# Kernel tuning notes

Measured on AMD Instinct MI355X. Metric: run time of the kernel, lower is better.

The kernel has to match this reference:

```python
import jax, jax.numpy as jnp
import numpy as np

EPS = 1e-12  # matches torch F.normalize eps

def _l2norm(v, axis):
    n = jnp.sqrt(jnp.sum(v * v, axis=axis, keepdims=True))
    return v / jnp.maximum(n, EPS)

def setup_inputs() -> dict:
    key = jax.random.key(0)
    k1, k2, k3 = jax.random.split(key, 3)
    N, D, H, W, K = 64, 128, 60, 80, 64
    x = jax.random.normal(k1, (N, D, H, W), dtype=jnp.float32)
    conv_w = jax.random.normal(k2, (K, D), dtype=jnp.float32) * 0.1
    centroids = jax.random.uniform(k3, (K, D), dtype=jnp.float32)
    return {"x": x, "conv_w": conv_w, "centroids": centroids}

def reference(x, conv_w, centroids):
    N, D, H, W = x.shape
    K = conv_w.shape[0]
    # descriptor-wise L2 normalization over channel dim
    x = _l2norm(x, axis=1)
    xf = x.reshape(N, D, H * W)                       # [N, D, P]
    # 1x1 conv (no bias) == matmul over channels, then softmax over clusters
    logits = jnp.einsum('kd,ndp->nkp', conv_w, xf)    # [N, K, P]
    sa = jax.nn.softmax(logits, axis=1)               # [N, K, P]
    # vlad[n,k,:] = sum_p sa[n,k,p] * (xf[n,:,p] - centroids[k])
    agg = jnp.einsum('nkp,ndp->nkd', sa, xf)          # [N, K, D]
    vlad = agg - sa.sum(axis=-1)[..., None] * centroids[None]
    vlad = _l2norm(vlad, axis=2)                      # intra-normalization
    vlad = vlad.reshape(N, K * D)
    vlad = _l2norm(vlad, axis=1)                      # global L2 norm
    return vlad
```

## Files before the change

### kernel.cpp

```cpp
#include <hip/hip_runtime.h>
#include <math.h>

#define NN 64
#define DD 128
#define PP 4800
#define KK 64
#define BPN 15
#define PB  320
#define CP  64
#define NCH 5

#define WT  136
#define XPT 136
#define XDT 88
#define SAT 88

typedef __attribute__((ext_vector_type(8))) short bf16x8;
typedef __attribute__((ext_vector_type(4))) float f32x4;

__device__ __forceinline__ unsigned short f2bf(float f) {
  unsigned u = __float_as_uint(f);
  u += 0x7fffu + ((u >> 16) & 1u);
  return (unsigned short)(u >> 16);
}
__device__ __forceinline__ float bf2f(unsigned short s) {
  return __uint_as_float(((unsigned)s) << 16);
}

template <bool ATOMIC>
__global__ __launch_bounds__(256, 2) void main_kernel(const float* __restrict__ x,
                                                      const float* __restrict__ conv_w,
                                                      float* __restrict__ pagg,
                                                      float* __restrict__ pssum) {
  __shared__ __align__(16) unsigned short w_s[KK * WT];
  __shared__ __align__(16) unsigned short xpd[CP * XPT];
  __shared__ __align__(16) unsigned short xdp[DD * XDT];
  __shared__ __align__(16) unsigned short sa_s[KK * SAT];
  __shared__ float invn_s[CP];
  __shared__ float ssred[256];

  const int b = blockIdx.x;
  const int n = b / BPN;
  const int sl = b % BPN;
  const int t = threadIdx.x;
  const int lane = t & 63;
  const int wv = t >> 6;
  const int lq = lane >> 4;
  const int ll = lane & 15;

  {
    int k = t >> 2, h = t & 3;
    const float4* wp = (const float4*)(conv_w + k * DD + h * 32);
    unsigned short* dst = &w_s[k * WT + h * 32];
#pragma unroll
    for (int i = 0; i < 4; ++i) {
      float4 a = wp[2 * i], c = wp[2 * i + 1];
      bf16x8 o = {(short)f2bf(a.x), (short)f2bf(a.y), (short)f2bf(a.z), (short)f2bf(a.w),
                  (short)f2bf(c.x), (short)f2bf(c.y), (short)f2bf(c.z), (short)f2bf(c.w)};
      *(bf16x8*)&dst[8 * i] = o;
    }
  }

  f32x4 acc[8];
#pragma unroll
  for (int i = 0; i < 8; ++i) acc[i] = (f32x4){0.f, 0.f, 0.f, 0.f};
  float ssacc[16];
#pragma unroll
  for (int i = 0; i < 16; ++i) ssacc[i] = 0.f;

  for (int c = 0; c < NCH; ++c) {
    const int p0 = sl * PB + c * CP;
    __syncthreads();

    {
      int d = t >> 1, h = t & 1;
      const float4* xp = (const float4*)(x + ((size_t)n * DD + d) * PP + p0 + h * 32);
      unsigned short* xdrow = &xdp[d * XDT + h * 32];
#pragma unroll
      for (int i = 0; i < 4; ++i) {
        float4 a = xp[2 * i], c2 = xp[2 * i + 1];
        unsigned short e0 = f2bf(a.x), e1 = f2bf(a.y), e2 = f2bf(a.z), e3 = f2bf(a.w);
        unsigned short e4 = f2bf(c2.x), e5 = f2bf(c2.y), e6 = f2bf(c2.z), e7 = f2bf(c2.w);
        bf16x8 o = {(short)e0, (short)e1, (short)e2, (short)e3,
                    (short)e4, (short)e5, (short)e6, (short)e7};
        *(bf16x8*)&xdrow[8 * i] = o;
        int pl = h * 32 + 8 * i;
        xpd[(pl + 0) * XPT + d] = e0;
        xpd[(pl + 1) * XPT + d] = e1;
        xpd[(pl + 2) * XPT + d] = e2;
        xpd[(pl + 3) * XPT + d] = e3;
        xpd[(pl + 4) * XPT + d] = e4;
        xpd[(pl + 5) * XPT + d] = e5;
        xpd[(pl + 6) * XPT + d] = e6;
        xpd[(pl + 7) * XPT + d] = e7;
      }
    }
    __syncthreads();

    if (t < 128) {
      int p = t >> 1, hh = t & 1;
      const unsigned short* row = &xpd[p * XPT + hh * 64];
      float s = 0.f;
#pragma unroll
      for (int i = 0; i < 8; ++i) {
        bf16x8 v = *(const bf16x8*)&row[8 * i];
#pragma unroll
        for (int j = 0; j < 8; ++j) {
          float f = bf2f((unsigned short)v[j]);
          s = fmaf(f, f, s);
        }
      }
      s += __shfl_xor(s, 1);
      if (hh == 0) invn_s[p] = 1.0f / fmaxf(sqrtf(s), 1e-12f);
    }
    __syncthreads();

    {
      f32x4 lg[4];
#pragma unroll
      for (int kt = 0; kt < 4; ++kt) lg[kt] = (f32x4){0.f, 0.f, 0.f, 0.f};
#pragma unroll
      for (int ks = 0; ks < 4; ++ks) {
        bf16x8 bfrag = *(const bf16x8*)&xpd[(wv * 16 + ll) * XPT + ks * 32 + lq * 8];
#pragma unroll
        for (int kt = 0; kt < 4; ++kt) {
          bf16x8 afrag = *(const bf16x8*)&w_s[(kt * 16 + ll) * WT + ks * 32 + lq * 8];
          lg[kt] = __builtin_amdgcn_mfma_f32_16x16x32_bf16(afrag, bfrag, lg[kt], 0, 0, 0);
        }
      }
      float iv = invn_s[wv * 16 + ll];
      float vals[16];
      float m = -1e30f;
#pragma unroll
      for (int kt = 0; kt < 4; ++kt)
#pragma unroll
        for (int r = 0; r < 4; ++r) {
          float v = lg[kt][r] * iv;
          vals[kt * 4 + r] = v;
          m = fmaxf(m, v);
        }
      m = fmaxf(m, __shfl_xor(m, 16));
      m = fmaxf(m, __shfl_xor(m, 32));
      float se = 0.f;
#pragma unroll
      for (int i = 0; i < 16; ++i) {
        float e = __expf(vals[i] - m);
        vals[i] = e;
        se += e;
      }
      se += __shfl_xor(se, 16);
      se += __shfl_xor(se, 32);
      float rinv = 1.0f / se;
      float r2 = rinv * iv;
#pragma unroll
      for (int kt = 0; kt < 4; ++kt)
#pragma unroll
        for (int r = 0; r < 4; ++r) {
          float e = vals[kt * 4 + r];
          ssacc[kt * 4 + r] += e * rinv;
          sa_s[(kt * 16 + lq * 4 + r) * SAT + wv * 16 + ll] = f2bf(e * r2);
        }
    }
    __syncthreads();

#pragma unroll
    for (int ks = 0; ks < 2; ++ks) {
      bf16x8 afrag = *(const bf16x8*)&sa_s[(wv * 16 + ll) * SAT + ks * 32 + lq * 8];
#pragma unroll
      for (int dt = 0; dt < 8; ++dt) {
        bf16x8 bfrag = *(const bf16x8*)&xdp[(dt * 16 + ll) * XDT + ks * 32 + lq * 8];
        acc[dt] = __builtin_amdgcn_mfma_f32_16x16x32_bf16(afrag, bfrag, acc[dt], 0, 0, 0);
      }
    }
  }

  {
    size_t base = ATOMIC ? (size_t)n * (KK * DD) : (size_t)(n * BPN + sl) * (KK * DD);
#pragma unroll
    for (int dt = 0; dt < 8; ++dt)
#pragma unroll
      for (int r = 0; r < 4; ++r) {
        int off = (16 * wv + 4 * lq + r) * DD + dt * 16 + ll;
        if (ATOMIC)
          atomicAdd(&pagg[base + off], acc[dt][r]);
        else
          pagg[base + off] = acc[dt][r];
      }
  }
#pragma unroll
  for (int i = 0; i < 16; ++i) {
    float s = ssacc[i];
    s += __shfl_xor(s, 1);
    s += __shfl_xor(s, 2);
    s += __shfl_xor(s, 4);
    s += __shfl_xor(s, 8);
    if (ll == 0) ssred[wv * 64 + (i >> 2) * 16 + lq * 4 + (i & 3)] = s;
  }
  __syncthreads();
  if (t < 64) {
    float s = ssred[t] + ssred[64 + t] + ssred[128 + t] + ssred[192 + t];
    if (ATOMIC)
      atomicAdd(&pssum[n * KK + t], s);
    else
      pssum[(n * BPN + sl) * KK + t] = s;
  }
}

__global__ __launch_bounds__(256) void epilogue_kernel(const float* __restrict__ pagg,
                                                       const float* __restrict__ pssum,
                                                       const float* __restrict__ cent,
                                                       float* __restrict__ out, int S) {
  __shared__ __align__(16) float agg_s[KK * 132];
  __shared__ float sred[KK];
  __shared__ float wsum[4];
  const int n = blockIdx.x, t = threadIdx.x;

#pragma unroll
  for (int it = 0; it < 8; ++it) {
    int idx = t + 256 * it;
    float4 a = {0.f, 0.f, 0.f, 0.f};
    for (int s = 0; s < S; ++s) {
      float4 v = ((const float4*)(pagg + (size_t)(n * S + s) * (KK * DD)))[idx];
      a.x += v.x; a.y += v.y; a.z += v.z; a.w += v.w;
    }
    int row = idx >> 5, col = (idx & 31) * 4;
    *(float4*)&agg_s[row * 132 + col] = a;
  }
  if (t < KK) {
    float s = 0.f;
    for (int ss = 0; ss < S; ++ss) s += pssum[(n * S + ss) * KK + t];
    sred[t] = s;
  }
  __syncthreads();

  const int k = t >> 2, j = t & 3;
  const float* ap = &agg_s[k * 132 + 32 * j];
  const float* cp = cent + (size_t)k * DD + 32 * j;
  const float sk = sred[k];

  float v[32];
  float ss = 0.f;
#pragma unroll
  for (int i = 0; i < 32; i += 4) {
    float4 a4 = *(const float4*)(ap + i);
    float4 c4 = *(const float4*)(cp + i);
    v[i + 0] = fmaf(-sk, c4.x, a4.x);
    v[i + 1] = fmaf(-sk, c4.y, a4.y);
    v[i + 2] = fmaf(-sk, c4.z, a4.z);
    v[i + 3] = fmaf(-sk, c4.w, a4.w);
    ss = fmaf(v[i + 0], v[i + 0], ss);
    ss = fmaf(v[i + 1], v[i + 1], ss);
    ss = fmaf(v[i + 2], v[i + 2], ss);
    ss = fmaf(v[i + 3], v[i + 3], ss);
  }
  ss += __shfl_xor(ss, 1);
  ss += __shfl_xor(ss, 2);
  float rinv = 1.0f / fmaxf(sqrtf(ss), 1e-12f);

  float gp = 0.f;
#pragma unroll
  for (int i = 0; i < 32; ++i) {
    v[i] *= rinv;
    gp = fmaf(v[i], v[i], gp);
  }
#pragma unroll
  for (int off = 1; off < 64; off <<= 1) gp += __shfl_xor(gp, off);
  if ((t & 63) == 0) wsum[t >> 6] = gp;
  __syncthreads();
  float g = wsum[0] + wsum[1] + wsum[2] + wsum[3];
  float ginv = 1.0f / fmaxf(sqrtf(g), 1e-12f);

  float* op = out + (size_t)n * KK * DD + (size_t)k * DD + 32 * j;
#pragma unroll
  for (int i = 0; i < 32; i += 4) {
    float4 o;
    o.x = v[i + 0] * ginv;
    o.y = v[i + 1] * ginv;
    o.z = v[i + 2] * ginv;
    o.w = v[i + 3] * ginv;
    *(float4*)(op + i) = o;
  }
}

extern "C" void kernel_launch(void* const* d_in, const int* in_sizes, int n_in,
                              void* d_out, int out_size, void* d_ws, size_t ws_size,
                              hipStream_t stream) {
  const float* x      = (const float*)d_in[0];
  const float* conv_w = (const float*)d_in[1];
  const float* cent   = (const float*)d_in[2];
  float* out = (float*)d_out;
  float* ws  = (float*)d_ws;

  const size_t need_partial =
      ((size_t)NN * BPN * KK * DD + (size_t)NN * BPN * KK) * sizeof(float);

  if (ws_size >= need_partial) {
    float* pagg  = ws;
    float* pssum = ws + (size_t)NN * BPN * KK * DD;
    main_kernel<false><<<NN * BPN, 256, 0, stream>>>(x, conv_w, pagg, pssum);
    epilogue_kernel<<<NN, 256, 0, stream>>>(pagg, pssum, cent, out, BPN);
  } else {
    float* pagg  = ws;
    float* pssum = ws + (size_t)NN * KK * DD;
    hipMemsetAsync(ws, 0, ((size_t)NN * KK * DD + (size_t)NN * KK) * sizeof(float), stream);
    main_kernel<true><<<NN * BPN, 256, 0, stream>>>(x, conv_w, pagg, pssum);
    epilogue_kernel<<<NN, 256, 0, stream>>>(pagg, pssum, cent, out, 1);
  }
}
```

Before: 277.1 us.

## Prefetch x chunks into registers, fuse norm computation, swizzle LDS, split epilogue

```diff
diff --git a/kernel.cpp b/kernel.cpp
--- a/kernel.cpp
+++ b/kernel.cpp
@@ -1,4 +1,5 @@
 #include <hip/hip_runtime.h>
+#include <hip/hip_bf16.h>
 #include <math.h>
 
 #define NN 64
@@ -12,8 +13,13 @@
 
 #define WT  136
 #define XPT 136
-#define XDT 88
-#define SAT 88
+#define XDT 72
+#define SAT 72
+
+#define PAGG_SZ  ((size_t)NN * BPN * KK * DD)
+#define PSSUM_SZ ((size_t)NN * BPN * KK)
+#define VTMP_SZ  ((size_t)NN * KK * DD)
+#define GSUM_SZ  ((size_t)NN * 8)
 
 typedef __attribute__((ext_vector_type(8))) short bf16x8;
 typedef __attribute__((ext_vector_type(4))) float f32x4;
@@ -23,11 +29,12 @@
   u += 0x7fffu + ((u >> 16) & 1u);
   return (unsigned short)(u >> 16);
 }
-__device__ __forceinline__ float bf2f(unsigned short s) {
-  return __uint_as_float(((unsigned)s) << 16);
-}
-
-template <bool ATOMIC>
+__device__ __forceinline__ unsigned pk2(float a, float b) {
+  union { __hip_bfloat162 h2; unsigned u; } cv;
+  cv.h2 = __float22bfloat162_rn(make_float2(a, b));
+  return cv.u;
+}
+
 __global__ __launch_bounds__(256, 2) void main_kernel(const float* __restrict__ x,
                                                       const float* __restrict__ conv_w,
                                                       float* __restrict__ pagg,
@@ -36,29 +43,35 @@
   __shared__ __align__(16) unsigned short xpd[CP * XPT];
   __shared__ __align__(16) unsigned short xdp[DD * XDT];
   __shared__ __align__(16) unsigned short sa_s[KK * SAT];
-  __shared__ float invn_s[CP];
-  __shared__ float ssred[256];
+  __shared__ float red_s[256];
 
   const int b = blockIdx.x;
-  const int n = b / BPN;
-  const int sl = b % BPN;
-  const int t = threadIdx.x;
-  const int lane = t & 63;
-  const int wv = t >> 6;
-  const int lq = lane >> 4;
-  const int ll = lane & 15;
+  const int n = b / BPN, sl = b % BPN;
+  const int t = threadIdx.x, lane = t & 63, wv = t >> 6;
+  const int lq = lane >> 4, ll = lane & 15;
+  const int pb = t & 7, db = t >> 3;
 
   {
     int k = t >> 2, h = t & 3;
-    const float4* wp = (const float4*)(conv_w + k * DD + h * 32);
+    const float* wp = conv_w + k * DD + h * 32;
     unsigned short* dst = &w_s[k * WT + h * 32];
 #pragma unroll
     for (int i = 0; i < 4; ++i) {
-      float4 a = wp[2 * i], c = wp[2 * i + 1];
-      bf16x8 o = {(short)f2bf(a.x), (short)f2bf(a.y), (short)f2bf(a.z), (short)f2bf(a.w),
-                  (short)f2bf(c.x), (short)f2bf(c.y), (short)f2bf(c.z), (short)f2bf(c.w)};
-      *(bf16x8*)&dst[8 * i] = o;
-    }
+      float4 a = *(const float4*)(wp + 8 * i);
+      float4 c = *(const float4*)(wp + 8 * i + 4);
+      uint4 o = {pk2(a.x, a.y), pk2(a.z, a.w), pk2(c.x, c.y), pk2(c.z, c.w)};
+      *(uint4*)&dst[8 * i] = o;
+    }
+  }
+  if (t < 64) red_s[t] = 0.f;
+
+  const float* xb = x + (size_t)n * DD * PP + (size_t)(4 * db) * PP + sl * PB + 8 * pb;
+
+  float4 pf[8];
+#pragma unroll
+  for (int r = 0; r < 4; ++r) {
+    pf[2 * r]     = *(const float4*)(xb + (size_t)r * PP);
+    pf[2 * r + 1] = *(const float4*)(xb + (size_t)r * PP + 4);
   }
 
   f32x4 acc[8];
@@ -69,66 +82,88 @@
   for (int i = 0; i < 16; ++i) ssacc[i] = 0.f;
 
   for (int c = 0; c < NCH; ++c) {
-    const int p0 = sl * PB + c * CP;
+    float4 cur[8];
+#pragma unroll
+    for (int i = 0; i < 8; ++i) cur[i] = pf[i];
+    if (c + 1 < NCH) {
+      const float* xc = xb + (c + 1) * CP;
+#pragma unroll
+      for (int r = 0; r < 4; ++r) {
+        pf[2 * r]     = *(const float4*)(xc + (size_t)r * PP);
+        pf[2 * r + 1] = *(const float4*)(xc + (size_t)r * PP + 4);
+      }
+    }
+
+    float sq[8];
+#pragma unroll
+    for (int h = 0; h < 2; ++h)
+#pragma unroll
+      for (int j = 0; j < 4; ++j) {
+        float s = 0.f;
+#pragma unroll
+        for (int r = 0; r < 4; ++r) {
+          float v = (&cur[2 * r + h].x)[j];
+          s = fmaf(v, v, s);
+        }
+        sq[4 * h + j] = s;
+      }
+#pragma unroll
+    for (int i = 0; i < 8; ++i) {
+      sq[i] += __shfl_xor(sq[i], 8);
+      sq[i] += __shfl_xor(sq[i], 16);
+      sq[i] += __shfl_xor(sq[i], 32);
+    }
+
     __syncthreads();
 
+    if (lane < 8) {
+#pragma unroll
+      for (int j = 0; j < 8; ++j) atomicAdd(&red_s[8 * lane + j], sq[j]);
+    }
+
     {
-      int d = t >> 1, h = t & 1;
-      const float4* xp = (const float4*)(x + ((size_t)n * DD + d) * PP + p0 + h * 32);
-      unsigned short* xdrow = &xdp[d * XDT + h * 32];
-#pragma unroll
-      for (int i = 0; i < 4; ++i) {
-        float4 a = xp[2 * i], c2 = xp[2 * i + 1];
-        unsigned short e0 = f2bf(a.x), e1 = f2bf(a.y), e2 = f2bf(a.z), e3 = f2bf(a.w);
-        unsigned short e4 = f2bf(c2.x), e5 = f2bf(c2.y), e6 = f2bf(c2.z), e7 = f2bf(c2.w);
-        bf16x8 o = {(short)e0, (short)e1, (short)e2, (short)e3,
-                    (short)e4, (short)e5, (short)e6, (short)e7};
-        *(bf16x8*)&xdrow[8 * i] = o;
-        int pl = h * 32 + 8 * i;
-        xpd[(pl + 0) * XPT + d] = e0;
-        xpd[(pl + 1) * XPT + d] = e1;
-        xpd[(pl + 2) * XPT + d] = e2;
-        xpd[(pl + 3) * XPT + d] = e3;
-        xpd[(pl + 4) * XPT + d] = e4;
-        xpd[(pl + 5) * XPT + d] = e5;
-        xpd[(pl + 6) * XPT + d] = e6;
-        xpd[(pl + 7) * XPT + d] = e7;
+      unsigned prow[4][4];
+#pragma unroll
+      for (int r = 0; r < 4; ++r) {
+        const float4& a = cur[2 * r];
+        const float4& c2 = cur[2 * r + 1];
+        prow[r][0] = pk2(a.x, a.y);
+        prow[r][1] = pk2(a.z, a.w);
+        prow[r][2] = pk2(c2.x, c2.y);
+        prow[r][3] = pk2(c2.z, c2.w);
+        uint4 o = {prow[r][0], prow[r][1], prow[r][2], prow[r][3]};
+        *(uint4*)&xdp[(4 * db + r) * XDT + 8 * pb] = o;
+      }
+      const int colh = (((db >> 1) ^ pb) << 3) + (db & 1) * 4;
+#pragma unroll
+      for (int j2 = 0; j2 < 4; ++j2) {
+        unsigned lo01 = __builtin_amdgcn_perm(prow[1][j2], prow[0][j2], 0x05040100u);
+        unsigned hi01 = __builtin_amdgcn_perm(prow[1][j2], prow[0][j2], 0x07060302u);
+        unsigned lo23 = __builtin_amdgcn_perm(prow[3][j2], prow[2][j2], 0x05040100u);
+        unsigned hi23 = __builtin_amdgcn_perm(prow[3][j2], prow[2][j2], 0x07060302u);
+        int p_e = 8 * pb + 2 * j2;
+        *(uint2*)&xpd[p_e * XPT + colh]       = make_uint2(lo01, lo23);
+        *(uint2*)&xpd[(p_e + 1) * XPT + colh] = make_uint2(hi01, hi23);
       }
     }
     __syncthreads();
 
-    if (t < 128) {
-      int p = t >> 1, hh = t & 1;
-      const unsigned short* row = &xpd[p * XPT + hh * 64];
-      float s = 0.f;
-#pragma unroll
-      for (int i = 0; i < 8; ++i) {
-        bf16x8 v = *(const bf16x8*)&row[8 * i];
-#pragma unroll
-        for (int j = 0; j < 8; ++j) {
-          float f = bf2f((unsigned short)v[j]);
-          s = fmaf(f, f, s);
-        }
-      }
-      s += __shfl_xor(s, 1);
-      if (hh == 0) invn_s[p] = 1.0f / fmaxf(sqrtf(s), 1e-12f);
-    }
-    __syncthreads();
-
     {
+      const int prow_ = wv * 16 + ll;
+      const int swz = (2 * wv + (ll >> 3)) & 7;
       f32x4 lg[4];
 #pragma unroll
       for (int kt = 0; kt < 4; ++kt) lg[kt] = (f32x4){0.f, 0.f, 0.f, 0.f};
 #pragma unroll
       for (int ks = 0; ks < 4; ++ks) {
-        bf16x8 bfrag = *(const bf16x8*)&xpd[(wv * 16 + ll) * XPT + ks * 32 + lq * 8];
+        bf16x8 bfrag = *(const bf16x8*)&xpd[prow_ * XPT + ((((ks << 2) | lq) ^ swz) << 3)];
 #pragma unroll
         for (int kt = 0; kt < 4; ++kt) {
           bf16x8 afrag = *(const bf16x8*)&w_s[(kt * 16 + ll) * WT + ks * 32 + lq * 8];
           lg[kt] = __builtin_amdgcn_mfma_f32_16x16x32_bf16(afrag, bfrag, lg[kt], 0, 0, 0);
         }
       }
-      float iv = invn_s[wv * 16 + ll];
+      float iv = 1.0f / fmaxf(sqrtf(red_s[prow_]), 1e-12f);
       float vals[16];
       float m = -1e30f;
 #pragma unroll
@@ -158,10 +193,11 @@
         for (int r = 0; r < 4; ++r) {
           float e = vals[kt * 4 + r];
           ssacc[kt * 4 + r] += e * rinv;
-          sa_s[(kt * 16 + lq * 4 + r) * SAT + wv * 16 + ll] = f2bf(e * r2);
+          sa_s[(kt * 16 + lq * 4 + r) * SAT + prow_] = f2bf(e * r2);
         }
     }
     __syncthreads();
+    if (c + 1 < NCH && t < 64) red_s[t] = 0.f;
 
 #pragma unroll
     for (int ks = 0; ks < 2; ++ks) {
@@ -175,17 +211,12 @@
   }
 
   {
-    size_t base = ATOMIC ? (size_t)n * (KK * DD) : (size_t)(n * BPN + sl) * (KK * DD);
+    float* base = pagg + (size_t)(n * BPN + sl) * (KK * DD);
 #pragma unroll
     for (int dt = 0; dt < 8; ++dt)
 #pragma unroll
-      for (int r = 0; r < 4; ++r) {
-        int off = (16 * wv + 4 * lq + r) * DD + dt * 16 + ll;
-        if (ATOMIC)
-          atomicAdd(&pagg[base + off], acc[dt][r]);
-        else
-          pagg[base + off] = acc[dt][r];
-      }
+      for (int r = 0; r < 4; ++r)
+        base[(16 * wv + 4 * lq + r) * DD + dt * 16 + ll] = acc[dt][r];
   }
 #pragma unroll
   for (int i = 0; i < 16; ++i) {
@@ -194,91 +225,77 @@
     s += __shfl_xor(s, 2);
     s += __shfl_xor(s, 4);
     s += __shfl_xor(s, 8);
-    if (ll == 0) ssred[wv * 64 + (i >> 2) * 16 + lq * 4 + (i & 3)] = s;
+    if (ll == 0) red_s[wv * 64 + (i >> 2) * 16 + lq * 4 + (i & 3)] = s;
   }
   __syncthreads();
-  if (t < 64) {
-    float s = ssred[t] + ssred[64 + t] + ssred[128 + t] + ssred[192 + t];
-    if (ATOMIC)
-      atomicAdd(&pssum[n * KK + t], s);
-    else
-      pssum[(n * BPN + sl) * KK + t] = s;
-  }
-}
-
-__global__ __launch_bounds__(256) void epilogue_kernel(const float* __restrict__ pagg,
-                                                       const float* __restrict__ pssum,
-                                                       const float* __restrict__ cent,
-                                                       float* __restrict__ out, int S) {
-  __shared__ __align__(16) float agg_s[KK * 132];
-  __shared__ float sred[KK];
+  if (t < 64)
+    pssum[(n * BPN + sl) * KK + t] =
+        red_s[t] + red_s[64 + t] + red_s[128 + t] + red_s[192 + t];
+}
+
+__global__ __launch_bounds__(256) void ep1_kernel(const float* __restrict__ pagg,
+                                                  const float* __restrict__ pssum,
+                                                  const float* __restrict__ cent,
+                                                  float* __restrict__ vtmp,
+                                                  float* __restrict__ gsum) {
   __shared__ float wsum[4];
+  const int blk = blockIdx.x;
+  const int n = blk >> 3, kg = blk & 7;
+  const int t = threadIdx.x;
+  const int kl = t >> 5, c32 = t & 31;
+  const int k = kg * 8 + kl;
+  const size_t off = (size_t)k * DD + c32 * 4;
+
+  const float* base = pagg + (size_t)n * BPN * (KK * DD) + off;
+  float4 a = {0.f, 0.f, 0.f, 0.f};
+  for (int s = 0; s < BPN; ++s) {
+    float4 v = *(const float4*)(base + (size_t)s * (KK * DD));
+    a.x += v.x; a.y += v.y; a.z += v.z; a.w += v.w;
+  }
+  float sk = 0.f;
+  for (int s = 0; s < BPN; ++s) sk += pssum[(n * BPN + s) * KK + k];
+
+  float4 c4 = *(const float4*)(cent + off);
+  float4 v;
+  v.x = fmaf(-sk, c4.x, a.x);
+  v.y = fmaf(-sk, c4.y, a.y);
+  v.z = fmaf(-sk, c4.z, a.z);
+  v.w = fmaf(-sk, c4.w, a.w);
+
+  float pss = v.x * v.x + v.y * v.y + v.z * v.z + v.w * v.w;
+  float ss = pss;
+  ss += __shfl_xor(ss, 1);
+  ss += __shfl_xor(ss, 2);
+  ss += __shfl_xor(ss, 4);
+  ss += __shfl_xor(ss, 8);
+  ss += __shfl_xor(ss, 16);
+  float rinv = 1.0f / fmaxf(sqrtf(ss), 1e-12f);
+  v.x *= rinv; v.y *= rinv; v.z *= rinv; v.w *= rinv;
+  *(float4*)(vtmp + (size_t)n * (KK * DD) + off) = v;
+
+  float gp = pss * rinv * rinv;
+#pragma unroll
+  for (int o = 1; o < 64; o <<= 1) gp += __shfl_xor(gp, o);
+  if ((t & 63) == 0) wsum[t >> 6] = gp;
+  __syncthreads();
+  if (t == 0) gsum[blk] = wsum[0] + wsum[1] + wsum[2] + wsum[3];
+}
+
+__global__ __launch_bounds__(256) void ep2_kernel(const float* __restrict__ vtmp,
+                                                  const float* __restrict__ gsum,
+                                                  float* __restrict__ out) {
   const int n = blockIdx.x, t = threadIdx.x;
-
+  const float* gs = gsum + n * 8;
+  float g = gs[0] + gs[1] + gs[2] + gs[3] + gs[4] + gs[5] + gs[6] + gs[7];
+  float ginv = 1.0f / fmaxf(sqrtf(g), 1e-12f);
+  const float4* vi = (const float4*)(vtmp + (size_t)n * (KK * DD));
+  float4* vo = (float4*)(out + (size_t)n * (KK * DD));
 #pragma unroll
   for (int it = 0; it < 8; ++it) {
     int idx = t + 256 * it;
-    float4 a = {0.f, 0.f, 0.f, 0.f};
-    for (int s = 0; s < S; ++s) {
-      float4 v = ((const float4*)(pagg + (size_t)(n * S + s) * (KK * DD)))[idx];
-      a.x += v.x; a.y += v.y; a.z += v.z; a.w += v.w;
-    }
-    int row = idx >> 5, col = (idx & 31) * 4;
-    *(float4*)&agg_s[row * 132 + col] = a;
-  }
-  if (t < KK) {
-    float s = 0.f;
-    for (int ss = 0; ss < S; ++ss) s += pssum[(n * S + ss) * KK + t];
-    sred[t] = s;
-  }
-  __syncthreads();
-
-  const int k = t >> 2, j = t & 3;
-  const float* ap = &agg_s[k * 132 + 32 * j];
-  const float* cp = cent + (size_t)k * DD + 32 * j;
-  const float sk = sred[k];
-
-  float v[32];
-  float ss = 0.f;
-#pragma unroll
-  for (int i = 0; i < 32; i += 4) {
-    float4 a4 = *(const float4*)(ap + i);
-    float4 c4 = *(const float4*)(cp + i);
-    v[i + 0] = fmaf(-sk, c4.x, a4.x);
-    v[i + 1] = fmaf(-sk, c4.y, a4.y);
-    v[i + 2] = fmaf(-sk, c4.z, a4.z);
-    v[i + 3] = fmaf(-sk, c4.w, a4.w);
-    ss = fmaf(v[i + 0], v[i + 0], ss);
-    ss = fmaf(v[i + 1], v[i + 1], ss);
-    ss = fmaf(v[i + 2], v[i + 2], ss);
-    ss = fmaf(v[i + 3], v[i + 3], ss);
-  }
-  ss += __shfl_xor(ss, 1);
-  ss += __shfl_xor(ss, 2);
-  float rinv = 1.0f / fmaxf(sqrtf(ss), 1e-12f);
-
-  float gp = 0.f;
-#pragma unroll
-  for (int i = 0; i < 32; ++i) {
-    v[i] *= rinv;
-    gp = fmaf(v[i], v[i], gp);
-  }
-#pragma unroll
-  for (int off = 1; off < 64; off <<= 1) gp += __shfl_xor(gp, off);
-  if ((t & 63) == 0) wsum[t >> 6] = gp;
-  __syncthreads();
-  float g = wsum[0] + wsum[1] + wsum[2] + wsum[3];
-  float ginv = 1.0f / fmaxf(sqrtf(g), 1e-12f);
-
-  float* op = out + (size_t)n * KK * DD + (size_t)k * DD + 32 * j;
-#pragma unroll
-  for (int i = 0; i < 32; i += 4) {
-    float4 o;
-    o.x = v[i + 0] * ginv;
-    o.y = v[i + 1] * ginv;
-    o.z = v[i + 2] * ginv;
-    o.w = v[i + 3] * ginv;
-    *(float4*)(op + i) = o;
+    float4 f = vi[idx];
+    f.x *= ginv; f.y *= ginv; f.z *= ginv; f.w *= ginv;
+    vo[idx] = f;
   }
 }
 
@@ -291,19 +308,12 @@
   float* out = (float*)d_out;
   float* ws  = (float*)d_ws;
 
-  const size_t need_partial =
-      ((size_t)NN * BPN * KK * DD + (size_t)NN * BPN * KK) * sizeof(float);
-
-  if (ws_size >= need_partial) {
-    float* pagg  = ws;
-    float* pssum = ws + (size_t)NN * BPN * KK * DD;
-    main_kernel<false><<<NN * BPN, 256, 0, stream>>>(x, conv_w, pagg, pssum);
-    epilogue_kernel<<<NN, 256, 0, stream>>>(pagg, pssum, cent, out, BPN);
-  } else {
-    float* pagg  = ws;
-    float* pssum = ws + (size_t)NN * KK * DD;
-    hipMemsetAsync(ws, 0, ((size_t)NN * KK * DD + (size_t)NN * KK) * sizeof(float), stream);
-    main_kernel<true><<<NN * BPN, 256, 0, stream>>>(x, conv_w, pagg, pssum);
-    epilogue_kernel<<<NN, 256, 0, stream>>>(pagg, pssum, cent, out, 1);
-  }
-}
+  float* pagg  = ws;
+  float* pssum = pagg + PAGG_SZ;
+  float* vtmp  = pssum + PSSUM_SZ;
+  float* gsum  = vtmp + VTMP_SZ;
+
+  main_kernel<<<NN * BPN, 256, 0, stream>>>(x, conv_w, pagg, pssum);
+  ep1_kernel<<<NN * 8, 256, 0, stream>>>(pagg, pssum, cent, vtmp, gsum);
+  ep2_kernel<<<NN, 256, 0, stream>>>(vtmp, gsum, out);
+}
```

Result: faster. 246.8 us (-10.9%).
